# Performance work log

Measured on AMD Instinct MI355X. Metric: run time of the kernel, lower is better.

## Reference

```python
import jax, jax.numpy as jnp
import numpy as np


def setup_inputs() -> dict:
    key = jax.random.key(0)
    k1, k2 = jax.random.split(key)
    B, H, W, C = 8, 512, 512, 32
    img = jax.random.normal(k1, (B, H, W, C), dtype=jnp.float32)
    # normalized coords in [-1, 1]
    grid = jax.random.uniform(k2, (B, H, W, 2), dtype=jnp.float32, minval=-1.0, maxval=1.0)
    return {"img": img, "grid": grid}


def reference(img, grid):
    B, H, W, C = img.shape
    max_y = H - 1
    max_x = W - 1
    # unnormalize from [-1,1] to pixel coords
    x = 0.5 * ((grid[..., 0] + 1.0) * jnp.float32(max_x))
    y = 0.5 * ((grid[..., 1] + 1.0) * jnp.float32(max_y))

    x0 = jnp.floor(x).astype(jnp.int32)
    x1 = x0 + 1
    y0 = jnp.floor(y).astype(jnp.int32)
    y1 = y0 + 1

    x0c = jnp.clip(x0, 0, max_x)
    x1c = jnp.clip(x1, 0, max_x)
    y0c = jnp.clip(y0, 0, max_y)
    y1c = jnp.clip(y1, 0, max_y)

    b = jnp.arange(B, dtype=jnp.int32)[:, None, None]  # [B,1,1], broadcasts over grid HxW

    Ia = img[b, y0c, x0c]  # [B,Hg,Wg,C]
    Ib = img[b, y1c, x0c]
    Ic = img[b, y0c, x1c]
    Id = img[b, y1c, x1c]

    x0f = x0c.astype(jnp.float32)
    x1f = x1c.astype(jnp.float32)
    y0f = y0c.astype(jnp.float32)
    y1f = y1c.astype(jnp.float32)

    wa = ((x1f - x) * (y1f - y))[..., None]
    wb = ((x1f - x) * (y - y0f))[..., None]
    wc = ((x - x0f) * (y1f - y))[..., None]
    wd = ((x - x0f) * (y - y0f))[..., None]

    return wa * Ia + wb * Ib + wc * Ic + wd * Id
```

## Files before the change

### kernel.cpp

```cpp
#include <hip/hip_runtime.h>

__global__ __launch_bounds__(256) void Interpolate_86775519248465_kernel(
    const float* __restrict__ img,
    const float* __restrict__ grid,
    float* __restrict__ out)
{
    constexpr int W = 512;
    constexpr int C = 32;
    constexpr float MAXX = 511.0f;
    constexpr float MAXY = 511.0f;

    const unsigned gid = blockIdx.x * 256u + threadIdx.x;
    const unsigned pix = gid >> 3;
    const unsigned c   = (gid & 7u) << 2;

    const float2 g = *reinterpret_cast<const float2*>(grid + (size_t)pix * 2u);

    const float x = 0.5f * ((g.x + 1.0f) * MAXX);
    const float y = 0.5f * ((g.y + 1.0f) * MAXY);

    const int x0 = (int)floorf(x);
    const int y0 = (int)floorf(y);
    const int x1 = x0 + 1;
    const int y1 = y0 + 1;

    const int x0c = min(max(x0, 0), 511);
    const int x1c = min(max(x1, 0), 511);
    const int y0c = min(max(y0, 0), 511);
    const int y1c = min(max(y1, 0), 511);

    const float x0f = (float)x0c, x1f = (float)x1c;
    const float y0f = (float)y0c, y1f = (float)y1c;
    const float wa = (x1f - x) * (y1f - y);
    const float wb = (x1f - x) * (y - y0f);
    const float wc = (x - x0f) * (y1f - y);
    const float wd = (x - x0f) * (y - y0f);

    const unsigned b = pix >> 18;
    const size_t base = ((size_t)b << 18) * (size_t)C;

    const size_t ia = base + ((size_t)((unsigned)y0c * W + (unsigned)x0c) * C) + c;
    const size_t ib = base + ((size_t)((unsigned)y1c * W + (unsigned)x0c) * C) + c;
    const size_t ic = base + ((size_t)((unsigned)y0c * W + (unsigned)x1c) * C) + c;
    const size_t id = base + ((size_t)((unsigned)y1c * W + (unsigned)x1c) * C) + c;

    const float4 Ia = *reinterpret_cast<const float4*>(img + ia);
    const float4 Ib = *reinterpret_cast<const float4*>(img + ib);
    const float4 Ic = *reinterpret_cast<const float4*>(img + ic);
    const float4 Id = *reinterpret_cast<const float4*>(img + id);

    float4 o;
    o.x = wa * Ia.x + wb * Ib.x + wc * Ic.x + wd * Id.x;
    o.y = wa * Ia.y + wb * Ib.y + wc * Ic.y + wd * Id.y;
    o.z = wa * Ia.z + wb * Ib.z + wc * Ic.z + wd * Id.z;
    o.w = wa * Ia.w + wb * Ib.w + wc * Ic.w + wd * Id.w;

    *reinterpret_cast<float4*>(out + (size_t)pix * C + c) = o;
}

extern "C" void kernel_launch(void* const* d_in, const int* in_sizes, int n_in,
                              void* d_out, int out_size, void* d_ws, size_t ws_size,
                              hipStream_t stream) {
    const float* img  = (const float*)d_in[0];
    const float* grid = (const float*)d_in[1];
    float* out = (float*)d_out;

    const unsigned total = 8u * 512u * 512u * 8u;
    const unsigned block = 256u;
    const unsigned nblk = total / block;
    Interpolate_86775519248465_kernel<<<nblk, block, 0, stream>>>(img, grid, out);
}
```

Measured before the change: 500.0 us.

## Bin grid samples by image row band and XCD for cache-local gathers

Adds a binning pass that buckets each output pixel by batch and 32-row band of the source image and writes compact entries to workspace. An apply pass then maps each bin to one XCD, so each XCD's L2 sees a limited slice of the image and gather reuse goes up. Overflow pixels are computed directly, and there is a fallback to a direct kernel when workspace is too small. It costs extra passes, a memset, atomics and roughly 2x grid-sized entry traffic, and output writes become scattered.

```diff
diff --git a/kernel.cpp b/kernel.cpp
--- a/kernel.cpp
+++ b/kernel.cpp
@@ -1,61 +1,132 @@
 #include <hip/hip_runtime.h>
 
-__global__ __launch_bounds__(256) void Interpolate_86775519248465_kernel(
+
+#define NBINS 128u
+#define CAP   20480u
+#define ENT_OFF 4096
+
+__device__ __forceinline__ void bilinear_px(
+    const float* __restrict__ ibase,
+    float* __restrict__ out, unsigned pix, float x, float y, unsigned c)
+{
+    const int x0 = (int)floorf(x);
+    const int y0 = (int)floorf(y);
+    const int x0c = min(max(x0,     0), 511);
+    const int x1c = min(max(x0 + 1, 0), 511);
+    const int y0c = min(max(y0,     0), 511);
+    const int y1c = min(max(y0 + 1, 0), 511);
+
+    const float4 Ia = *reinterpret_cast<const float4*>(ibase + (unsigned)(y0c*512 + x0c)*32u + c);
+    const float4 Ic = *reinterpret_cast<const float4*>(ibase + (unsigned)(y0c*512 + x1c)*32u + c);
+    const float4 Ib = *reinterpret_cast<const float4*>(ibase + (unsigned)(y1c*512 + x0c)*32u + c);
+    const float4 Id = *reinterpret_cast<const float4*>(ibase + (unsigned)(y1c*512 + x1c)*32u + c);
+
+    const float wa = ((float)x1c - x) * ((float)y1c - y);
+    const float wb = ((float)x1c - x) * (y - (float)y0c);
+    const float wc = (x - (float)x0c) * ((float)y1c - y);
+    const float wd = (x - (float)x0c) * (y - (float)y0c);
+
+    float4 o;
+    o.x = wa*Ia.x + wb*Ib.x + wc*Ic.x + wd*Id.x;
+    o.y = wa*Ia.y + wb*Ib.y + wc*Ic.y + wd*Id.y;
+    o.z = wa*Ia.z + wb*Ib.z + wc*Ic.z + wd*Id.z;
+    o.w = wa*Ia.w + wb*Ib.w + wc*Ic.w + wd*Id.w;
+    *reinterpret_cast<float4*>(out + (size_t)pix*32u + c) = o;
+}
+
+__global__ __launch_bounds__(256) void gs_bin(
+    const float* __restrict__ grid,
+    const float* __restrict__ img,
+    float* __restrict__ out,
+    unsigned* __restrict__ gcnt,
+    float4* __restrict__ entries)
+{
+    __shared__ unsigned lcnt[16];
+    __shared__ unsigned lbase[16];
+    const unsigned tid = threadIdx.x;
+    if (tid < 16) lcnt[tid] = 0;
+    __syncthreads();
+
+    const unsigned blockbase = blockIdx.x << 10;
+    const unsigned batch = blockbase >> 18;
+
+    float xs[4], ys[4];
+    unsigned bandk[4], slotk[4], pixk[4];
+    #pragma unroll
+    for (int k = 0; k < 4; ++k) {
+        const unsigned pix = blockbase + tid + ((unsigned)k << 8);
+        const float2 g = *reinterpret_cast<const float2*>(grid + (size_t)pix * 2u);
+        const float x = 0.5f * ((g.x + 1.0f) * 511.0f);
+        const float y = 0.5f * ((g.y + 1.0f) * 511.0f);
+        const int y0 = (int)floorf(y);
+        const int y0c = min(max(y0, 0), 511);
+        const unsigned band = (unsigned)y0c >> 5;
+        slotk[k] = atomicAdd(&lcnt[band], 1u);
+        bandk[k] = band; pixk[k] = pix; xs[k] = x; ys[k] = y;
+    }
+    __syncthreads();
+    if (tid < 16) lbase[tid] = atomicAdd(&gcnt[batch * 16u + tid], lcnt[tid]);
+    __syncthreads();
+
+    const float* ibase = img + (((size_t)batch << 18) * 32u);
+    #pragma unroll
+    for (int k = 0; k < 4; ++k) {
+        const unsigned idx = lbase[bandk[k]] + slotk[k];
+        const unsigned bin = batch * 16u + bandk[k];
+        if (idx < CAP) {
+            float4 e;
+            e.x = xs[k]; e.y = ys[k];
+            e.z = __uint_as_float(pixk[k]); e.w = 0.0f;
+            entries[(size_t)bin * CAP + idx] = e;
+        } else {
+            for (unsigned c = 0; c < 32; c += 4)
+                bilinear_px(ibase, out, pixk[k], xs[k], ys[k], c);
+        }
+    }
+}
+
+__global__ __launch_bounds__(256) void gs_apply(
+    const float* __restrict__ img,
+    float* __restrict__ out,
+    const unsigned* __restrict__ gcnt,
+    const float4* __restrict__ entries)
+{
+    const unsigned bid = blockIdx.x;
+    const unsigned xcd      = bid & 7u;
+    const unsigned j        = bid >> 3;
+    const unsigned ord      = j >> 9;
+    const unsigned blkInBin = j & 511u;
+    const unsigned bin   = ord * 8u + xcd;
+    const unsigned batch = bin >> 4;
+
+    unsigned n = gcnt[bin];
+    if (n > CAP) n = CAP;
+
+    const unsigned tid = threadIdx.x;
+    const unsigned grp = tid >> 3;
+    const unsigned c   = (tid & 7u) << 2;
+    const float* ibase = img + (((size_t)batch << 18) * 32u);
+
+    for (unsigned p = blkInBin * 32u + grp; p < n; p += 16384u) {
+        const float4 e = entries[(size_t)bin * CAP + p];
+        bilinear_px(ibase, out, __float_as_uint(e.z), e.x, e.y, c);
+    }
+}
+
+__global__ __launch_bounds__(256) void gs_direct(
     const float* __restrict__ img,
     const float* __restrict__ grid,
     float* __restrict__ out)
 {
-    constexpr int W = 512;
-    constexpr int C = 32;
-    constexpr float MAXX = 511.0f;
-    constexpr float MAXY = 511.0f;
-
     const unsigned gid = blockIdx.x * 256u + threadIdx.x;
     const unsigned pix = gid >> 3;
     const unsigned c   = (gid & 7u) << 2;
-
     const float2 g = *reinterpret_cast<const float2*>(grid + (size_t)pix * 2u);
-
-    const float x = 0.5f * ((g.x + 1.0f) * MAXX);
-    const float y = 0.5f * ((g.y + 1.0f) * MAXY);
-
-    const int x0 = (int)floorf(x);
-    const int y0 = (int)floorf(y);
-    const int x1 = x0 + 1;
-    const int y1 = y0 + 1;
-
-    const int x0c = min(max(x0, 0), 511);
-    const int x1c = min(max(x1, 0), 511);
-    const int y0c = min(max(y0, 0), 511);
-    const int y1c = min(max(y1, 0), 511);
-
-    const float x0f = (float)x0c, x1f = (float)x1c;
-    const float y0f = (float)y0c, y1f = (float)y1c;
-    const float wa = (x1f - x) * (y1f - y);
-    const float wb = (x1f - x) * (y - y0f);
-    const float wc = (x - x0f) * (y1f - y);
-    const float wd = (x - x0f) * (y - y0f);
-
-    const unsigned b = pix >> 18;
-    const size_t base = ((size_t)b << 18) * (size_t)C;
-
-    const size_t ia = base + ((size_t)((unsigned)y0c * W + (unsigned)x0c) * C) + c;
-    const size_t ib = base + ((size_t)((unsigned)y1c * W + (unsigned)x0c) * C) + c;
-    const size_t ic = base + ((size_t)((unsigned)y0c * W + (unsigned)x1c) * C) + c;
-    const size_t id = base + ((size_t)((unsigned)y1c * W + (unsigned)x1c) * C) + c;
-
-    const float4 Ia = *reinterpret_cast<const float4*>(img + ia);
-    const float4 Ib = *reinterpret_cast<const float4*>(img + ib);
-    const float4 Ic = *reinterpret_cast<const float4*>(img + ic);
-    const float4 Id = *reinterpret_cast<const float4*>(img + id);
-
-    float4 o;
-    o.x = wa * Ia.x + wb * Ib.x + wc * Ic.x + wd * Id.x;
-    o.y = wa * Ia.y + wb * Ib.y + wc * Ic.y + wd * Id.y;
-    o.z = wa * Ia.z + wb * Ib.z + wc * Ic.z + wd * Id.z;
-    o.w = wa * Ia.w + wb * Ib.w + wc * Ic.w + wd * Id.w;
-
-    *reinterpret_cast<float4*>(out + (size_t)pix * C + c) = o;
+    const float x = 0.5f * ((g.x + 1.0f) * 511.0f);
+    const float y = 0.5f * ((g.y + 1.0f) * 511.0f);
+    const unsigned batch = pix >> 18;
+    const float* ibase = img + (((size_t)batch << 18) * 32u);
+    bilinear_px(ibase, out, pix, x, y, c);
 }
 
 extern "C" void kernel_launch(void* const* d_in, const int* in_sizes, int n_in,
@@ -65,8 +136,14 @@
     const float* grid = (const float*)d_in[1];
     float* out = (float*)d_out;
 
-    const unsigned total = 8u * 512u * 512u * 8u;
-    const unsigned block = 256u;
-    const unsigned nblk = total / block;
-    Interpolate_86775519248465_kernel<<<nblk, block, 0, stream>>>(img, grid, out);
+    const size_t need = (size_t)ENT_OFF + (size_t)NBINS * CAP * sizeof(float4);
+    if (d_ws != nullptr && ws_size >= need) {
+        unsigned* gcnt  = (unsigned*)d_ws;
+        float4* entries = (float4*)((char*)d_ws + ENT_OFF);
+        hipMemsetAsync(gcnt, 0, NBINS * sizeof(unsigned), stream);
+        gs_bin<<<2048, 256, 0, stream>>>(grid, img, out, gcnt, entries);
+        gs_apply<<<65536, 256, 0, stream>>>(img, out, gcnt, entries);
+    } else {
+        gs_direct<<<65536, 256, 0, stream>>>(img, grid, out);
+    }
 }
```

Measured after the change: 501.8 us. About the same (+0.4%).
